# Optimization experiments

Hardware: AMD Instinct MI355X
Metric: run time of the kernel (lower is better)

Reference implementation:

```python
import jax, jax.numpy as jnp
import numpy as np
from jax import lax

B, N, C, FH, FW = 2, 6, 64, 16, 44
D = 64
DEPTH_MIN, DEPTH_MAX = 1.0, 60.0
IMG_H, IMG_W = 256, 704
BEV_H, BEV_W = 128, 128
XMIN, XMAX = -51.2, 51.2
YMIN, YMAX = -51.2, 51.2
BN_EPS = 1e-5


def _make_cameras():
    fx = fy = 557.0
    K = np.array([[fx, 0.0, IMG_W / 2.0], [0.0, fy, IMG_H / 2.0], [0.0, 0.0, 1.0]], np.float32)
    intr = np.broadcast_to(K, (B, N, 3, 3)).copy()
    extr = np.zeros((B, N, 4, 4), np.float32)
    for n in range(N):
        c, s = np.cos(2 * np.pi * n / N), np.sin(2 * np.pi * n / N)
        # columns = [right, down, forward] of camera expressed in ego frame
        Rc = np.array([[s, 0.0, c], [-c, 0.0, s], [0.0, -1.0, 0.0]], np.float32)
        extr[:, n, :3, :3] = Rc
        extr[:, n, :3, 3] = np.array([c, s, 1.5], np.float32)
        extr[:, n, 3, 3] = 1.0
    return jnp.asarray(intr), jnp.asarray(extr)


def _frustum():
    # (D, FH, FW, 3) holding (u*d, v*d, d) in original-image pixel coords
    ds = jnp.linspace(DEPTH_MIN, DEPTH_MAX, D)[:, None, None]
    xs = jnp.linspace(0.0, IMG_W - 1.0, FW)[None, None, :]
    ys = jnp.linspace(0.0, IMG_H - 1.0, FH)[None, :, None]
    d = jnp.broadcast_to(ds, (D, FH, FW))
    x = jnp.broadcast_to(xs, (D, FH, FW))
    y = jnp.broadcast_to(ys, (D, FH, FW))
    return jnp.stack([x * d, y * d, d], axis=-1)


def _conv(x, w, b, pad):
    y = lax.conv_general_dilated(x, w, (1, 1), pad, dimension_numbers=("NCHW", "OIHW", "NCHW"))
    return y + b[None, :, None, None]


def setup_inputs() -> dict:
    key = jax.random.key(0)
    k0, k1, k2 = jax.random.split(key, 3)
    intr, extr = _make_cameras()
    return {
        "features": jax.random.normal(k0, (B, N, C, FH, FW), jnp.float32),
        "intrinsics": intr,
        "extrinsics": extr,
        "conv1_w": jax.random.normal(k1, (C, C, 3, 3), jnp.float32) / np.sqrt(C * 9.0).astype(np.float32),
        "conv1_b": jnp.zeros((C,), jnp.float32),
        "bn_gamma": jnp.ones((C,), jnp.float32),
        "bn_beta": jnp.zeros((C,), jnp.float32),
        "bn_mean": jnp.zeros((C,), jnp.float32),
        "bn_var": jnp.ones((C,), jnp.float32),
        "conv2_w": jax.random.normal(k2, (D, C, 1, 1), jnp.float32) / np.sqrt(float(C)).astype(np.float32),
        "conv2_b": jnp.zeros((D,), jnp.float32),
    }


def reference(features, intrinsics, extrinsics, conv1_w, conv1_b, bn_gamma, bn_beta, bn_mean, bn_var, conv2_w, conv2_b):
    Bv, Nv, Cv, fH, fW = features.shape
    x = features.reshape(Bv * Nv, Cv, fH, fW)

    # DepthNet: conv3x3 -> BN (inference form) -> ReLU -> conv1x1 -> softmax over depth bins
    h = _conv(x, conv1_w, conv1_b, "SAME")
    scale = (bn_gamma / jnp.sqrt(bn_var + BN_EPS))[None, :, None, None]
    h = (h - bn_mean[None, :, None, None]) * scale + bn_beta[None, :, None, None]
    h = jax.nn.relu(h)
    depth = jax.nn.softmax(_conv(h, conv2_w, conv2_b, "VALID"), axis=1)  # (B*N, D, fH, fW)

    # Lift: outer product of features with depth distribution
    volume = x[:, :, None] * depth[:, None]  # (B*N, C, D, fH, fW)

    # Unproject frustum to ego frame for every camera
    pts = _frustum()  # (D, fH, fW, 3)
    Kinv = jnp.linalg.inv(intrinsics)  # (B, N, 3, 3)
    cam = jnp.einsum("bnij,dhwj->bndhwi", Kinv, pts)
    R = extrinsics[..., :3, :3]
    t = extrinsics[..., :3, 3]
    ego = jnp.einsum("bnij,bndhwj->bndhwi", R, cam) + t[:, :, None, None, None, :]

    # BEV voxel indices; invalid points routed to an overflow bucket that is dropped
    ix = jnp.floor((ego[..., 0] - XMIN) / (XMAX - XMIN) * BEV_W).astype(jnp.int32)
    iy = jnp.floor((ego[..., 1] - YMIN) / (YMAX - YMIN) * BEV_H).astype(jnp.int32)
    valid = (ix >= 0) & (ix < BEV_W) & (iy >= 0) & (iy < BEV_H)
    idx = jnp.where(valid, iy * BEV_W + ix, BEV_H * BEV_W)  # (B, N, D, fH, fW)

    # Splat: scatter-add over all cameras/depths/pixels per batch element
    vol = volume.reshape(Bv, Nv, Cv, -1).transpose(0, 2, 1, 3).reshape(Bv, Cv, -1)  # (B, C, N*D*fH*fW)
    idxb = idx.reshape(Bv, -1)

    def pool(v, i):
        return jnp.zeros((Cv, BEV_H * BEV_W + 1), v.dtype).at[:, i].add(v)[:, :-1]

    return jax.vmap(pool)(vol, idxb).reshape(Bv, Cv, BEV_H, BEV_W)
```

## Files before the change

### kernel.cpp

```cpp
#include <hip/hip_runtime.h>
#include <hip/hip_bf16.h>
#include <math.h>

#define B_  2
#define N_  6
#define C_  64
#define FH_ 16
#define FW_ 44
#define D_  64
#define PIX (FH_*FW_)
#define BNI (B_*N_)
#define NPILLAR (BNI*PIX)
#define NPOINT (NPILLAR*D_)
#define BEVH 128
#define BEVW 128
#define BEVC (BEVH*BEVW)
#define NCELL (B_*BEVC)
#define PW 46
#define PP (18*PW)

typedef unsigned int u32;

__device__ __forceinline__ int rlane_i(int v, int l) {
    return __builtin_amdgcn_readlane(v, l);
}
__device__ __forceinline__ float rlane_f(float v, int l) {
    return __int_as_float(__builtin_amdgcn_readlane(__float_as_int(v), l));
}

__global__ __launch_bounds__(256) void k_init_conv(const float* __restrict__ feat,
                                                   const float* __restrict__ w1,
                                                   float* __restrict__ hpAll,
                                                   float* __restrict__ x_t,
                                                   const float* __restrict__ w2,
                                                   float* __restrict__ w2t,
                                                   u32* __restrict__ counts,
                                                   u32* __restrict__ gcursor,
                                                   const float* __restrict__ intr,
                                                   const float* __restrict__ extr,
                                                   double* __restrict__ Mbuf) {
    const int blk = blockIdx.x;
    const int tid = threadIdx.x;

    __shared__ float smem[16 * PP];

    if (blk < 768) {
        if (blk < 128) counts[blk * 256 + tid] = 0u;

        const int bn = blk >> 6;
        const int ch = (blk >> 4) & 3;
        const int o0 = (blk & 15) * 4;
        const int c0 = ch * 16;

        for (int t = tid; t < 4 * PP; t += 256)
            ((float4*)smem)[t] = make_float4(0.f, 0.f, 0.f, 0.f);
        __syncthreads();

        const float4* fb4 = (const float4*)(feat + ((size_t)bn * C_ + c0) * PIX);
#pragma unroll
        for (int k = 0; k < 11; ++k) {
            const int j = k * 256 + tid;
            const int pl = j / 176;
            const int r  = j % 176;
            const int row = r / 11, q = r % 11;
            const float4 v = fb4[j];
            float* dstp = &smem[pl * PP + (row + 1) * PW + q * 4 + 1];
            dstp[0] = v.x; dstp[1] = v.y; dstp[2] = v.z; dstp[3] = v.w;
        }
        __syncthreads();

        const int y0 = tid / FW_,          x0 = tid % FW_;
        const int y1 = (tid + 256) / FW_,  x1 = (tid + 256) % FW_;
        const int y2 = (tid + 512) / FW_,  x2 = (tid + 512) % FW_;
        const int rp0 = y0 * PW + x0;
        const int rp1 = y1 * PW + x1;
        const int rp2 = y2 * PW + x2;

        float a00=0,a01=0,a02=0,a03=0, a10=0,a11=0,a12=0,a13=0,
              a20=0,a21=0,a22=0,a23=0;
#pragma unroll 4
        for (int i = 0; i < 16; ++i) {
            const float* wr0 = w1 + ((size_t)(o0 + 0) * C_ + c0 + i) * 9;
            const float* wr1 = w1 + ((size_t)(o0 + 1) * C_ + c0 + i) * 9;
            const float* wr2 = w1 + ((size_t)(o0 + 2) * C_ + c0 + i) * 9;
            const float* wr3 = w1 + ((size_t)(o0 + 3) * C_ + c0 + i) * 9;
            const float* pb = &smem[i * PP];
#define CONV_SLOT(RP, A0, A1, A2, A3)                                          \
    {                                                                          \
        const float* bb = pb + (RP);                                           \
        const float n0=bb[0], n1=bb[1], n2=bb[2];                              \
        const float n3=bb[PW], n4=bb[PW+1], n5=bb[PW+2];                       \
        const float n6=bb[2*PW], n7=bb[2*PW+1], n8=bb[2*PW+2];                 \
        A0 += n0*wr0[0]+n1*wr0[1]+n2*wr0[2]+n3*wr0[3]+n4*wr0[4]                \
            + n5*wr0[5]+n6*wr0[6]+n7*wr0[7]+n8*wr0[8];                         \
        A1 += n0*wr1[0]+n1*wr1[1]+n2*wr1[2]+n3*wr1[3]+n4*wr1[4]                \
            + n5*wr1[5]+n6*wr1[6]+n7*wr1[7]+n8*wr1[8];                         \
        A2 += n0*wr2[0]+n1*wr2[1]+n2*wr2[2]+n3*wr2[3]+n4*wr2[4]                \
            + n5*wr2[5]+n6*wr2[6]+n7*wr2[7]+n8*wr2[8];                         \
        A3 += n0*wr3[0]+n1*wr3[1]+n2*wr3[2]+n3*wr3[3]+n4*wr3[4]                \
            + n5*wr3[5]+n6*wr3[6]+n7*wr3[7]+n8*wr3[8];                         \
    }
            CONV_SLOT(rp0, a00, a01, a02, a03);
            CONV_SLOT(rp1, a10, a11, a12, a13);
            if (tid < PIX - 512) CONV_SLOT(rp2, a20, a21, a22, a23);
#undef CONV_SLOT
        }
        float* hp = hpAll + (size_t)ch * NPOINT + (size_t)bn * PIX * C_;
        *(float4*)&hp[(size_t)tid * C_ + o0]         = make_float4(a00,a01,a02,a03);
        *(float4*)&hp[(size_t)(tid + 256) * C_ + o0] = make_float4(a10,a11,a12,a13);
        if (tid < PIX - 512)
            *(float4*)&hp[(size_t)(tid + 512) * C_ + o0] = make_float4(a20,a21,a22,a23);
    } else if (blk < 900) {
        const int u  = blk - 768;
        const int bn = u / 11;
        const int p0 = (u % 11) * 64;
        const int lane = tid & 63;
        const int row4 = tid >> 6;
        float* tile = smem;
#pragma unroll
        for (int k = 0; k < 16; ++k) {
            const int c = k * 4 + row4;
            tile[c * 65 + lane] = feat[((size_t)bn * C_ + c) * PIX + p0 + lane];
        }
        __syncthreads();
#pragma unroll
        for (int k = 0; k < 16; ++k) {
            const int r = k * 4 + row4;
            x_t[((size_t)bn * PIX + p0 + r) * C_ + lane] = tile[lane * 65 + r];
        }
    } else {
#pragma unroll
        for (int k = 0; k < 16; ++k) {
            const int idx = k * 256 + tid;
            const int d = idx >> 6, c = idx & 63;
            w2t[c * D_ + d] = w2[idx];
        }
        if (tid == 0) *gcursor = 0u;
        if (tid < BNI) {
            const float* K = &intr[tid * 9];
            const double a00 = K[0], a01 = K[1], a02 = K[2];
            const double a10 = K[3], a11 = K[4], a12 = K[5];
            const double a20 = K[6], a21 = K[7], a22 = K[8];
            const double det = a00 * (a11 * a22 - a12 * a21)
                             - a01 * (a10 * a22 - a12 * a20)
                             + a02 * (a10 * a21 - a11 * a20);
            const double id = 1.0 / det;
            double inv[9];
            inv[0] = (a11 * a22 - a12 * a21) * id;
            inv[1] = (a02 * a21 - a01 * a22) * id;
            inv[2] = (a01 * a12 - a02 * a11) * id;
            inv[3] = (a12 * a20 - a10 * a22) * id;
            inv[4] = (a00 * a22 - a02 * a20) * id;
            inv[5] = (a02 * a10 - a00 * a12) * id;
            inv[6] = (a10 * a21 - a11 * a20) * id;
            inv[7] = (a01 * a20 - a00 * a21) * id;
            inv[8] = (a00 * a11 - a01 * a10) * id;
            const float* E = &extr[tid * 16];
            double* M = &Mbuf[tid * 9];
            for (int r = 0; r < 3; ++r) {
                const double r0 = E[r*4+0], r1 = E[r*4+1], r2 = E[r*4+2];
                M[r*3+0] = r0*inv[0] + r1*inv[3] + r2*inv[6];
                M[r*3+1] = r0*inv[1] + r1*inv[4] + r2*inv[7];
                M[r*3+2] = r0*inv[2] + r1*inv[5] + r2*inv[8];
            }
        }
    }
}

__global__ __launch_bounds__(256) void k_depth(const float* __restrict__ hpAll,
                                               const float* __restrict__ b1,
                                               const float* __restrict__ gma,
                                               const float* __restrict__ bta,
                                               const float* __restrict__ mu,
                                               const float* __restrict__ var,
                                               const float* __restrict__ w2t,
                                               const float* __restrict__ b2,
                                               const double* __restrict__ Mbuf,
                                               const float* __restrict__ extr,
                                               uint2* __restrict__ pc,
                                               u32* __restrict__ counts) {
    const int tid  = threadIdx.x;
    const int wv   = tid >> 6;
    const int lane = tid & 63;
    const int pillar = blockIdx.x * 4 + wv;
    const int bn = pillar / PIX;
    const int p  = pillar % PIX;
    const int yi = p / FW_;
    const int xi = p % FW_;

    __shared__ float w2s[C_ * D_];
#pragma unroll
    for (int k = 0; k < 4; ++k)
        ((float4*)w2s)[k * 256 + tid] = ((const float4*)w2t)[k * 256 + tid];

    float h;
    {
        const size_t o = (size_t)pillar * C_ + lane;
        h = hpAll[o] + hpAll[NPOINT + o] + hpAll[2 * (size_t)NPOINT + o]
          + hpAll[3 * (size_t)NPOINT + o] + b1[lane];
        const float sc = gma[lane] / sqrtf(var[lane] + 1e-5f);
        h = (h - mu[lane]) * sc + bta[lane];
        h = h > 0.f ? h : 0.f;
    }
    __syncthreads();

    float l0 = 0.f, l1 = 0.f, l2 = 0.f, l3 = 0.f;
#pragma unroll
    for (int c = 0; c < C_; c += 4) {
        l0 += rlane_f(h, c + 0) * w2s[(c + 0) * D_ + lane];
        l1 += rlane_f(h, c + 1) * w2s[(c + 1) * D_ + lane];
        l2 += rlane_f(h, c + 2) * w2s[(c + 2) * D_ + lane];
        l3 += rlane_f(h, c + 3) * w2s[(c + 3) * D_ + lane];
    }
    const float logit = b2[lane] + ((l0 + l1) + (l2 + l3));

    float m = logit;
#pragma unroll
    for (int off = 32; off; off >>= 1) m = fmaxf(m, __shfl_xor(m, off));
    float e = expf(logit - m);
    float s = e;
#pragma unroll
    for (int off = 32; off; off >>= 1) s += __shfl_xor(s, off);

    const double* M = &Mbuf[bn * 9];
    const double xn = (double)xi * (703.0 / 43.0);
    const double yn = (double)yi * 17.0;
    const double vx = M[0] * xn + M[1] * yn + M[2];
    const double vy = M[3] * xn + M[4] * yn + M[5];
    const double dd = 1.0 + (double)lane * (59.0 / 63.0);
    const float* E = &extr[bn * 16];
    const double ex = dd * vx + (double)E[3];
    const double ey = dd * vy + (double)E[7];
    const int ix = (int)floor((ex + 51.2) * 1.25);
    const int iy = (int)floor((ey + 51.2) * 1.25);
    const bool valid = (ix >= 0) && (ix < BEVW) && (iy >= 0) && (iy < BEVH);

    const int i = pillar * D_ + lane;
    uint2 rec;
    rec.x = __float_as_uint(e / s);
    if (valid) {
        const int cell = (bn / N_) * BEVC + iy * BEVW + ix;
        const u32 rank = atomicAdd(&counts[cell], 1u);
        rec.y = (rank << 15) | (u32)cell;
    } else {
        rec.y = 0xFFFFFFFFu;
    }
    pc[i] = rec;
}

__global__ __launch_bounds__(256) void k_alloc(const u32* __restrict__ counts,
                                               u32* __restrict__ offs,
                                               u32* __restrict__ gcursor) {
    const int cell = blockIdx.x * 256 + threadIdx.x;
    const int lane = threadIdx.x & 63;
    const u32 len = counts[cell];
    u32 incl = len;
#pragma unroll
    for (int off = 1; off < 64; off <<= 1) {
        u32 t = __shfl_up(incl, off);
        if (lane >= off) incl += t;
    }
    u32 base = 0;
    if (lane == 63) base = atomicAdd(gcursor, incl);
    base = (u32)__shfl((int)base, 63);
    offs[cell] = base + incl - len;
}

__global__ __launch_bounds__(256) void k_zero_place(const uint2* __restrict__ pc,
                                                    const u32* __restrict__ offs,
                                                    const u32* __restrict__ counts,
                                                    const u32* __restrict__ gcursor,
                                                    uint2* __restrict__ sorted,
                                                    u32* __restrict__ offs_end,
                                                    float* __restrict__ spool) {
    const int blk = blockIdx.x;
    const int tid = threadIdx.x;
    if (blk < 2048) {
        const int gt = blk * 256 + tid;
        const int cell = gt >> 4;
        const int q    = gt & 15;
        const u32 n = counts[cell];
        const u32 s = offs[cell];
        const bool needzero = (n == 0u) || ((s >> 6) != ((s + n - 1) >> 6));
        if (needzero)
            *(float4*)&spool[(size_t)cell * C_ + q * 4] =
                make_float4(0.f, 0.f, 0.f, 0.f);
    } else if (blk < 4160) {
        const int i = (blk - 2048) * 256 + tid;
        const uint2 rec = pc[i];
        if (rec.y != 0xFFFFFFFFu) {
            const u32 cell = rec.y & 0x7FFFu;
            const u32 rank = rec.y >> 15;
            const u32 pos  = offs[cell] + rank;
            uint2 o; o.x = rec.x; o.y = (cell << 14) | (u32)(i >> 6);
            sorted[pos] = o;
        }
    } else {
        const u32 total = *gcursor;
        if (tid < 128) {
            uint2 dummy; dummy.x = 0u; dummy.y = 0xFFFFFFFFu;
            sorted[total + tid] = dummy;
        }
        if (tid == 128) *offs_end = total;
    }
}

__global__ __launch_bounds__(256) void k_pool(const uint2* __restrict__ sorted,
                                              const u32* __restrict__ offsets,
                                              const float* __restrict__ x_t,
                                              float* __restrict__ spool) {
    const u32 P = offsets[NCELL];
    const int wv   = threadIdx.x >> 6;
    const int lane = threadIdx.x & 63;
    const u32 j0   = ((u32)blockIdx.x * 4u + (u32)wv) * 64u;
    if (j0 >= P) return;

    const uint2 pr  = sorted[j0 + (u32)lane];
    const float myw = __uint_as_float(pr.x);
    const int mycell = (int)(pr.y >> 14);
    int mypil = (int)(pr.y & 0x3FFFu);
    if (mypil >= NPILLAR) mypil = 0;

    const int prev_cell = (j0 > 0) ? (int)(sorted[j0 - 1].y >> 14) : -1;
    const int next_cell = (int)(sorted[j0 + 64].y >> 14);

    const int upc = __shfl_up(mycell, 1);
    const unsigned long long bm = __ballot(lane == 0 || mycell != upc);

    float xr[8];
#pragma unroll
    for (int t = 0; t < 8; ++t)
        xr[t] = x_t[(size_t)rlane_i(mypil, t) * C_ + lane];

    float acc = 0.f;
    bool first = true;

#pragma unroll
    for (int t = 0; t < 64; ++t) {
        acc += rlane_f(myw, t) * xr[t & 7];
        if (t + 8 < 64)
            xr[t & 7] = x_t[(size_t)rlane_i(mypil, t + 8) * C_ + lane];
        const bool flush = (t == 63) || ((bm >> (t + 1)) & 1ull);
        if (flush) {
            const int cc = rlane_i(mycell, t);
            if (cc < NCELL) {
                float* dst = spool + (size_t)cc * C_ + lane;
                const bool spans = (first && cc == prev_cell)
                                || (t == 63 && next_cell == cc);
                if (spans) atomicAdd(dst, acc);
                else *dst = acc;
            }
            acc = 0.f;
            first = false;
        }
    }
}

__global__ __launch_bounds__(256) void k_out(const float* __restrict__ spool,
                                             float* __restrict__ out) {
    const int tile_i = blockIdx.x;
    const int b  = tile_i >> 8;
    const int c0 = (tile_i & 255) * 64;
    const int tid = threadIdx.x;
    const int lane = tid & 63;
    const int row4 = tid >> 6;

    __shared__ float tile[64][65];
#pragma unroll
    for (int k = 0; k < 16; ++k) {
        const int r = k * 4 + row4;
        tile[r][lane] = spool[((size_t)b * BEVC + c0 + r) * C_ + lane];
    }
    __syncthreads();
#pragma unroll
    for (int k = 0; k < 16; ++k) {
        const int ch = k * 4 + row4;
        out[((size_t)b * C_ + ch) * BEVC + c0 + lane] = tile[lane][ch];
    }
}

extern "C" void kernel_launch(void* const* d_in, const int* in_sizes, int n_in,
                              void* d_out, int out_size, void* d_ws, size_t ws_size,
                              hipStream_t stream) {
    const float* feat  = (const float*)d_in[0];
    const float* intr  = (const float*)d_in[1];
    const float* extr  = (const float*)d_in[2];
    const float* w1    = (const float*)d_in[3];
    const float* b1    = (const float*)d_in[4];
    const float* gma   = (const float*)d_in[5];
    const float* bta   = (const float*)d_in[6];
    const float* mu    = (const float*)d_in[7];
    const float* var   = (const float*)d_in[8];
    const float* w2    = (const float*)d_in[9];
    const float* b2    = (const float*)d_in[10];
    float* out = (float*)d_out;

    double* Mbuf    = (double*)d_ws;
    u32*    gcursor = (u32*)((char*)d_ws + 960);
    uint2*  sorted  = (uint2*)((char*)d_ws + 1024);
    uint2*  pc      = sorted + NPOINT + 128;
    float*  x_t     = (float*)(pc + NPOINT);
    float*  hpAll   = x_t + NPOINT;
    u32*    counts  = (u32*)(hpAll + 4 * (size_t)NPOINT);
    u32*    offs    = counts + NCELL;
    float*  w2t     = (float*)(offs + NCELL + 1);

    float*  spool   = hpAll;

    k_init_conv<<<901, 256, 0, stream>>>(feat, w1, hpAll, x_t, w2, w2t,
                                         counts, gcursor, intr, extr, Mbuf);
    k_depth<<<NPILLAR / 4, 256, 0, stream>>>(hpAll, b1, gma, bta, mu, var,
                                             w2t, b2, Mbuf, extr, pc, counts);
    k_alloc<<<NCELL / 256, 256, 0, stream>>>(counts, offs, gcursor);
    k_zero_place<<<4161, 256, 0, stream>>>(pc, offs, counts, gcursor,
                                           sorted, &offs[NCELL], spool);
    k_pool<<<NPOINT / 64 / 4, 256, 0, stream>>>(sorted, offs, x_t, spool);
    k_out<<<512, 256, 0, stream>>>(spool, out);

    (void)in_sizes; (void)n_in; (void)ws_size; (void)out_size;
}
```

Baseline: 89.13 us.

## Replace counting-sort pooling with direct atomic scatter fused into depth kernel

The separate counting, prefix allocation, placement and segmented-pooling kernels are removed. The depth kernel now computes each point's softmax weight and BEV cell, then atomically adds weight times feature straight into the pooled grid. Zeroing of the pool buffer moves into extra blocks of the init kernel, and the pool buffer gets its own region in the workspace. This saves three launches and the sort traffic, but adds up to 64 float atomics per lane per pillar, with contention wherever many points fall into the same cell.

```diff
diff --git a/kernel.cpp b/kernel.cpp
--- a/kernel.cpp
+++ b/kernel.cpp
@@ -34,8 +34,7 @@
                                                    float* __restrict__ x_t,
                                                    const float* __restrict__ w2,
                                                    float* __restrict__ w2t,
-                                                   u32* __restrict__ counts,
-                                                   u32* __restrict__ gcursor,
+                                                   float* __restrict__ spool,
                                                    const float* __restrict__ intr,
                                                    const float* __restrict__ extr,
                                                    double* __restrict__ Mbuf) {
@@ -45,8 +44,6 @@
     __shared__ float smem[16 * PP];
 
     if (blk < 768) {
-        if (blk < 128) counts[blk * 256 + tid] = 0u;
-
         const int bn = blk >> 6;
         const int ch = (blk >> 4) & 3;
         const int o0 = (blk & 15) * 4;
@@ -128,14 +125,13 @@
             const int r = k * 4 + row4;
             x_t[((size_t)bn * PIX + p0 + r) * C_ + lane] = tile[lane * 65 + r];
         }
-    } else {
+    } else if (blk == 900) {
 #pragma unroll
         for (int k = 0; k < 16; ++k) {
             const int idx = k * 256 + tid;
             const int d = idx >> 6, c = idx & 63;
             w2t[c * D_ + d] = w2[idx];
         }
-        if (tid == 0) *gcursor = 0u;
         if (tid < BNI) {
             const float* K = &intr[tid * 9];
             const double a00 = K[0], a01 = K[1], a02 = K[2];
@@ -164,21 +160,27 @@
                 M[r*3+2] = r0*inv[2] + r1*inv[5] + r2*inv[8];
             }
         }
-    }
-}
-
-__global__ __launch_bounds__(256) void k_depth(const float* __restrict__ hpAll,
-                                               const float* __restrict__ b1,
-                                               const float* __restrict__ gma,
-                                               const float* __restrict__ bta,
-                                               const float* __restrict__ mu,
-                                               const float* __restrict__ var,
-                                               const float* __restrict__ w2t,
-                                               const float* __restrict__ b2,
-                                               const double* __restrict__ Mbuf,
-                                               const float* __restrict__ extr,
-                                               uint2* __restrict__ pc,
-                                               u32* __restrict__ counts) {
+    } else {
+        const int u = blk - 901;
+        float4* sp4 = (float4*)spool;
+#pragma unroll
+        for (int k = 0; k < 16; ++k)
+            sp4[(size_t)u * 4096 + k * 256 + tid] = make_float4(0.f, 0.f, 0.f, 0.f);
+    }
+}
+
+__global__ __launch_bounds__(256) void k_depth_scatter(const float* __restrict__ hpAll,
+                                                       const float* __restrict__ b1,
+                                                       const float* __restrict__ gma,
+                                                       const float* __restrict__ bta,
+                                                       const float* __restrict__ mu,
+                                                       const float* __restrict__ var,
+                                                       const float* __restrict__ w2t,
+                                                       const float* __restrict__ b2,
+                                                       const double* __restrict__ Mbuf,
+                                                       const float* __restrict__ extr,
+                                                       const float* __restrict__ x_t,
+                                                       float* __restrict__ spool) {
     const int tid  = threadIdx.x;
     const int wv   = tid >> 6;
     const int lane = tid & 63;
@@ -221,6 +223,7 @@
     float s = e;
 #pragma unroll
     for (int off = 32; off; off >>= 1) s += __shfl_xor(s, off);
+    const float wval = e / s;
 
     const double* M = &Mbuf[bn * 9];
     const double xn = (double)xi * (703.0 / 43.0);
@@ -234,124 +237,16 @@
     const int ix = (int)floor((ex + 51.2) * 1.25);
     const int iy = (int)floor((ey + 51.2) * 1.25);
     const bool valid = (ix >= 0) && (ix < BEVW) && (iy >= 0) && (iy < BEVH);
-
-    const int i = pillar * D_ + lane;
-    uint2 rec;
-    rec.x = __float_as_uint(e / s);
-    if (valid) {
-        const int cell = (bn / N_) * BEVC + iy * BEVW + ix;
-        const u32 rank = atomicAdd(&counts[cell], 1u);
-        rec.y = (rank << 15) | (u32)cell;
-    } else {
-        rec.y = 0xFFFFFFFFu;
-    }
-    pc[i] = rec;
-}
-
-__global__ __launch_bounds__(256) void k_alloc(const u32* __restrict__ counts,
-                                               u32* __restrict__ offs,
-                                               u32* __restrict__ gcursor) {
-    const int cell = blockIdx.x * 256 + threadIdx.x;
-    const int lane = threadIdx.x & 63;
-    const u32 len = counts[cell];
-    u32 incl = len;
-#pragma unroll
-    for (int off = 1; off < 64; off <<= 1) {
-        u32 t = __shfl_up(incl, off);
-        if (lane >= off) incl += t;
-    }
-    u32 base = 0;
-    if (lane == 63) base = atomicAdd(gcursor, incl);
-    base = (u32)__shfl((int)base, 63);
-    offs[cell] = base + incl - len;
-}
-
-__global__ __launch_bounds__(256) void k_zero_place(const uint2* __restrict__ pc,
-                                                    const u32* __restrict__ offs,
-                                                    const u32* __restrict__ counts,
-                                                    const u32* __restrict__ gcursor,
-                                                    uint2* __restrict__ sorted,
-                                                    u32* __restrict__ offs_end,
-                                                    float* __restrict__ spool) {
-    const int blk = blockIdx.x;
-    const int tid = threadIdx.x;
-    if (blk < 2048) {
-        const int gt = blk * 256 + tid;
-        const int cell = gt >> 4;
-        const int q    = gt & 15;
-        const u32 n = counts[cell];
-        const u32 s = offs[cell];
-        const bool needzero = (n == 0u) || ((s >> 6) != ((s + n - 1) >> 6));
-        if (needzero)
-            *(float4*)&spool[(size_t)cell * C_ + q * 4] =
-                make_float4(0.f, 0.f, 0.f, 0.f);
-    } else if (blk < 4160) {
-        const int i = (blk - 2048) * 256 + tid;
-        const uint2 rec = pc[i];
-        if (rec.y != 0xFFFFFFFFu) {
-            const u32 cell = rec.y & 0x7FFFu;
-            const u32 rank = rec.y >> 15;
-            const u32 pos  = offs[cell] + rank;
-            uint2 o; o.x = rec.x; o.y = (cell << 14) | (u32)(i >> 6);
-            sorted[pos] = o;
-        }
-    } else {
-        const u32 total = *gcursor;
-        if (tid < 128) {
-            uint2 dummy; dummy.x = 0u; dummy.y = 0xFFFFFFFFu;
-            sorted[total + tid] = dummy;
-        }
-        if (tid == 128) *offs_end = total;
-    }
-}
-
-__global__ __launch_bounds__(256) void k_pool(const uint2* __restrict__ sorted,
-                                              const u32* __restrict__ offsets,
-                                              const float* __restrict__ x_t,
-                                              float* __restrict__ spool) {
-    const u32 P = offsets[NCELL];
-    const int wv   = threadIdx.x >> 6;
-    const int lane = threadIdx.x & 63;
-    const u32 j0   = ((u32)blockIdx.x * 4u + (u32)wv) * 64u;
-    if (j0 >= P) return;
-
-    const uint2 pr  = sorted[j0 + (u32)lane];
-    const float myw = __uint_as_float(pr.x);
-    const int mycell = (int)(pr.y >> 14);
-    int mypil = (int)(pr.y & 0x3FFFu);
-    if (mypil >= NPILLAR) mypil = 0;
-
-    const int prev_cell = (j0 > 0) ? (int)(sorted[j0 - 1].y >> 14) : -1;
-    const int next_cell = (int)(sorted[j0 + 64].y >> 14);
-
-    const int upc = __shfl_up(mycell, 1);
-    const unsigned long long bm = __ballot(lane == 0 || mycell != upc);
-
-    float xr[8];
-#pragma unroll
-    for (int t = 0; t < 8; ++t)
-        xr[t] = x_t[(size_t)rlane_i(mypil, t) * C_ + lane];
-
-    float acc = 0.f;
-    bool first = true;
-
-#pragma unroll
+    const int cellv = valid ? ((bn / N_) * BEVC + iy * BEVW + ix) : -1;
+
+    const float xv = x_t[(size_t)pillar * C_ + lane];
+
+#pragma unroll 8
     for (int t = 0; t < 64; ++t) {
-        acc += rlane_f(myw, t) * xr[t & 7];
-        if (t + 8 < 64)
-            xr[t & 7] = x_t[(size_t)rlane_i(mypil, t + 8) * C_ + lane];
-        const bool flush = (t == 63) || ((bm >> (t + 1)) & 1ull);
-        if (flush) {
-            const int cc = rlane_i(mycell, t);
-            if (cc < NCELL) {
-                float* dst = spool + (size_t)cc * C_ + lane;
-                const bool spans = (first && cc == prev_cell)
-                                || (t == 63 && next_cell == cc);
-                if (spans) atomicAdd(dst, acc);
-                else *dst = acc;
-            }
-            acc = 0.f;
-            first = false;
+        const int cc = rlane_i(cellv, t);
+        if (cc >= 0) {
+            const float wt = rlane_f(wval, t);
+            atomicAdd(&spool[(size_t)cc * C_ + lane], wt * xv);
         }
     }
 }
@@ -395,26 +290,17 @@
     const float* b2    = (const float*)d_in[10];
     float* out = (float*)d_out;
 
-    double* Mbuf    = (double*)d_ws;
-    u32*    gcursor = (u32*)((char*)d_ws + 960);
-    uint2*  sorted  = (uint2*)((char*)d_ws + 1024);
-    uint2*  pc      = sorted + NPOINT + 128;
-    float*  x_t     = (float*)(pc + NPOINT);
-    float*  hpAll   = x_t + NPOINT;
-    u32*    counts  = (u32*)(hpAll + 4 * (size_t)NPOINT);
-    u32*    offs    = counts + NCELL;
-    float*  w2t     = (float*)(offs + NCELL + 1);
-
-    float*  spool   = hpAll;
-
-    k_init_conv<<<901, 256, 0, stream>>>(feat, w1, hpAll, x_t, w2, w2t,
-                                         counts, gcursor, intr, extr, Mbuf);
-    k_depth<<<NPILLAR / 4, 256, 0, stream>>>(hpAll, b1, gma, bta, mu, var,
-                                             w2t, b2, Mbuf, extr, pc, counts);
-    k_alloc<<<NCELL / 256, 256, 0, stream>>>(counts, offs, gcursor);
-    k_zero_place<<<4161, 256, 0, stream>>>(pc, offs, counts, gcursor,
-                                           sorted, &offs[NCELL], spool);
-    k_pool<<<NPOINT / 64 / 4, 256, 0, stream>>>(sorted, offs, x_t, spool);
+    double* Mbuf  = (double*)d_ws;
+    float*  x_t   = (float*)((char*)d_ws + 1024);
+    float*  hpAll = x_t + NPOINT;
+    float*  spool = hpAll + 4 * (size_t)NPOINT;
+    float*  w2t   = spool + (size_t)NCELL * C_;
+
+    k_init_conv<<<1029, 256, 0, stream>>>(feat, w1, hpAll, x_t, w2, w2t,
+                                          spool, intr, extr, Mbuf);
+    k_depth_scatter<<<NPILLAR / 4, 256, 0, stream>>>(hpAll, b1, gma, bta, mu,
+                                                     var, w2t, b2, Mbuf, extr,
+                                                     x_t, spool);
     k_out<<<512, 256, 0, stream>>>(spool, out);
 
     (void)in_sizes; (void)n_in; (void)ws_size; (void)out_size;
```

Measured after the change: 179.9 us. 102% more time.
